# Performance work log

Measured on AMD Instinct MI355X. Metric: run time of the kernel, lower is better.

The kernel has to match this reference:

```python
import jax, jax.numpy as jnp
import numpy as np

N_NODES = 100000


def _gcn_layer(x, W, src, dst, w):
    # GCNConv(add_self_loops=False, normalize=False, bias=False):
    # h = x @ W; out[i] = sum_{e: dst[e]=i} w[e] * h[src[e]]
    h = x @ W                                   # [N, nhid]
    msgs = h[src] * w[:, None]                  # [E, nhid] gather + scale
    return jax.ops.segment_sum(msgs, dst, num_segments=N_NODES)  # scatter-add


def setup_inputs() -> dict:
    key = jax.random.key(0)
    ks = jax.random.split(key, 7)
    N, E, P, F, H = N_NODES, 1000000, 500000, 128, 64
    x = jax.random.normal(ks[0], (N, F), dtype=jnp.float32)
    edge_index = jax.random.randint(ks[1], (2, E), 0, N, dtype=jnp.int64)
    edge_weight = jax.random.uniform(ks[2], (E,), dtype=jnp.float32)
    pos_edge_index = jax.random.randint(ks[3], (2, P), 0, N, dtype=jnp.int64)
    W1 = jax.random.normal(ks[4], (F, H), dtype=jnp.float32) * (1.0 / np.sqrt(F))
    W2 = jax.random.normal(ks[5], (H, H), dtype=jnp.float32) * (1.0 / np.sqrt(H))
    Wlin = jax.random.normal(ks[6], (2, 2 * H), dtype=jnp.float32) * (1.0 / np.sqrt(2 * H))
    return {"x": x, "edge_index": edge_index, "edge_weight": edge_weight,
            "pos_edge_index": pos_edge_index, "W1": W1, "W2": W2, "Wlin": Wlin}


def reference(x, edge_index, edge_weight, pos_edge_index, W1, W2, Wlin):
    src, dst = edge_index[0], edge_index[1]
    h = jax.nn.relu(_gcn_layer(x, W1, src, dst, edge_weight))   # conv1 + relu
    z = _gcn_layer(h, W2, src, dst, edge_weight)                # conv2
    # decode: gather endpoint embeddings, concat, linear (no bias)
    pairs = jnp.concatenate([z[pos_edge_index[0]], z[pos_edge_index[1]]], axis=1)  # [P, 2H]
    return pairs @ Wlin.T                                       # [P, 2]
```

## Files before the change

kernel.cpp:

```cpp
#include <hip/hip_runtime.h>

#define F_IN 128
#define H_DIM 64
#define NBUCK_MAX 1024
#define BCAP 1664

typedef short s16x8 __attribute__((ext_vector_type(8)));
typedef float f32x4 __attribute__((ext_vector_type(4)));
typedef float f32x2 __attribute__((ext_vector_type(2)));

union FragU {
    s16x8 s;
    uint4 q;
    unsigned short u[8];
};

__device__ __forceinline__ unsigned short f2bf(float f) {
    unsigned int b = __float_as_uint(f);
    b += 0x7fffu + ((b >> 16) & 1u);
    return (unsigned short)(b >> 16);
}
__device__ __forceinline__ f32x2 up2(unsigned int v) {
    f32x2 r;
    r.x = __uint_as_float(v << 16);
    r.y = __uint_as_float(v & 0xffff0000u);
    return r;
}
__device__ __forceinline__ f32x2 fma2(f32x2 a, f32x2 b, f32x2 c) {
#if __has_builtin(__builtin_elementwise_fma)
    return __builtin_elementwise_fma(a, b, c);
#else
    f32x2 r;
    r.x = fmaf(a.x, b.x, c.x);
    r.y = fmaf(a.y, b.y, c.y);
    return r;
#endif
}

__device__ __forceinline__ void prepack_one(const float* __restrict__ W,
                                            unsigned short* __restrict__ wf, int KS, int tid) {
    int lane = tid & 63;
    int grp = tid >> 6;
    int ks = grp % KS;
    int ct = grp / KS;
    int col = ct * 16 + (lane & 15);
    int kbase = ks * 32 + (lane >> 4) * 8;
    FragU f;
#pragma unroll
    for (int j = 0; j < 8; ++j) f.u[j] = f2bf(W[(kbase + j) * H_DIM + col]);
    reinterpret_cast<uint4*>(wf)[tid] = f.q;
}

__global__ __launch_bounds__(256) void prepack_k(const float* __restrict__ W1, const float* __restrict__ W2,
                                                 unsigned short* __restrict__ wf1, unsigned short* __restrict__ wf2,
                                                 int* __restrict__ gcursor) {
    int tid = blockIdx.x * 256 + threadIdx.x;
    if (tid < NBUCK_MAX) gcursor[tid] = tid * BCAP;
    if (tid < 4 * 4 * 64) prepack_one(W1, wf1, 4, tid);
    else if (tid < 4 * 4 * 64 + 4 * 2 * 64) prepack_one(W2, wf2, 2, tid - 4 * 4 * 64);
}

__global__ __launch_bounds__(256) void gemm1_k(const float* __restrict__ x,
                                               const unsigned short* __restrict__ wf,
                                               unsigned short* __restrict__ outb, int N) {
    constexpr int KS = F_IN / 32;
    int wv = threadIdx.x >> 6;
    int lane = threadIdx.x & 63;
    int rb = blockIdx.x * 64 + wv * 16;
    int ra = rb + (lane & 15);
    if (ra > N - 1) ra = N - 1;
    int koct = lane >> 4;

    FragU af[KS];
    const float* ap = x + (size_t)ra * F_IN + koct * 8;
#pragma unroll
    for (int ks = 0; ks < KS; ++ks) {
        float4 v0 = *reinterpret_cast<const float4*>(ap + ks * 32);
        float4 v1 = *reinterpret_cast<const float4*>(ap + ks * 32 + 4);
        af[ks].u[0] = f2bf(v0.x); af[ks].u[1] = f2bf(v0.y);
        af[ks].u[2] = f2bf(v0.z); af[ks].u[3] = f2bf(v0.w);
        af[ks].u[4] = f2bf(v1.x); af[ks].u[5] = f2bf(v1.y);
        af[ks].u[6] = f2bf(v1.z); af[ks].u[7] = f2bf(v1.w);
    }

    const uint4* bq = reinterpret_cast<const uint4*>(wf);
    f32x4 acc[4];
#pragma unroll
    for (int ct = 0; ct < 4; ++ct) acc[ct] = (f32x4){0.f, 0.f, 0.f, 0.f};
#pragma unroll
    for (int ct = 0; ct < 4; ++ct) {
#pragma unroll
        for (int ks = 0; ks < KS; ++ks) {
            FragU b;
            b.q = bq[(ct * KS + ks) * 64 + lane];
            acc[ct] = __builtin_amdgcn_mfma_f32_16x16x32_bf16(af[ks].s, b.s, acc[ct], 0, 0, 0);
        }
    }

    int ro_base = rb + (lane >> 4) * 4;
    int col = lane & 15;
#pragma unroll
    for (int ct = 0; ct < 4; ++ct) {
#pragma unroll
        for (int j = 0; j < 4; ++j) {
            int ro = ro_base + j;
            if (ro < N) outb[(size_t)ro * H_DIM + ct * 16 + col] = f2bf(acc[ct][j]);
        }
    }
}

__global__ __launch_bounds__(256) void gemm2v_k(const unsigned short* __restrict__ a1b,
                                                const unsigned short* __restrict__ wf,
                                                const float* __restrict__ Wlin,
                                                float4* __restrict__ uz, int N) {
    constexpr int KS = H_DIM / 32;
    int wv = threadIdx.x >> 6;
    int lane = threadIdx.x & 63;
    int rb = blockIdx.x * 64 + wv * 16;
    int ra = rb + (lane & 15);
    if (ra > N - 1) ra = N - 1;
    int koct = lane >> 4;

    FragU af[KS];
    const unsigned short* ap = a1b + (size_t)ra * H_DIM + koct * 8;
#pragma unroll
    for (int ks = 0; ks < KS; ++ks)
        af[ks].q = *reinterpret_cast<const uint4*>(ap + ks * 32);

    const uint4* bq = reinterpret_cast<const uint4*>(wf);
    f32x4 acc[4];
#pragma unroll
    for (int ct = 0; ct < 4; ++ct) acc[ct] = (f32x4){0.f, 0.f, 0.f, 0.f};
#pragma unroll
    for (int ct = 0; ct < 4; ++ct) {
#pragma unroll
        for (int ks = 0; ks < KS; ++ks) {
            FragU b;
            b.q = bq[(ct * KS + ks) * 64 + lane];
            acc[ct] = __builtin_amdgcn_mfma_f32_16x16x32_bf16(af[ks].s, b.s, acc[ct], 0, 0, 0);
        }
    }

    int c = lane & 15;
    float w0[4], w1[4], w2[4], w3[4];
#pragma unroll
    for (int ct = 0; ct < 4; ++ct) {
        int col = ct * 16 + c;
        w0[ct] = Wlin[col];
        w1[ct] = Wlin[128 + col];
        w2[ct] = Wlin[64 + col];
        w3[ct] = Wlin[192 + col];
    }
    int ro_base = rb + (lane >> 4) * 4;
#pragma unroll
    for (int j = 0; j < 4; ++j) {
        float p0 = 0.f, p1 = 0.f, p2 = 0.f, p3 = 0.f;
#pragma unroll
        for (int ct = 0; ct < 4; ++ct) {
            float zv = acc[ct][j];
            p0 = fmaf(zv, w0[ct], p0);
            p1 = fmaf(zv, w1[ct], p1);
            p2 = fmaf(zv, w2[ct], p2);
            p3 = fmaf(zv, w3[ct], p3);
        }
#pragma unroll
        for (int m = 1; m < 16; m <<= 1) {
            p0 += __shfl_xor(p0, m);
            p1 += __shfl_xor(p1, m);
            p2 += __shfl_xor(p2, m);
            p3 += __shfl_xor(p3, m);
        }
        int ro = ro_base + j;
        if (c == 0 && ro < N) uz[ro] = make_float4(p0, p1, p2, p3);
    }
}

__global__ __launch_bounds__(256) void binA_k(const int* __restrict__ ei, const float* __restrict__ ew,
                                              int* __restrict__ gcursor,
                                              unsigned long long* __restrict__ stage, int E, int nbuck) {
    __shared__ unsigned long long sstage[4096];
    __shared__ int smeta[4096];
    __shared__ int cnt[NBUCK_MAX];
    __shared__ int lbase[NBUCK_MAX];
    __shared__ int gbase[NBUCK_MAX];
    __shared__ int cur[NBUCK_MAX];
    __shared__ int wsum[256];
    int tid = threadIdx.x;
    int e0 = blockIdx.x * 4096;
    int ecount = min(4096, E - e0);
    for (int i = tid; i < nbuck; i += 256) { cnt[i] = 0; cur[i] = 0; }
    __syncthreads();
    for (int i = tid; i < ecount; i += 256)
        atomicAdd(&cnt[ei[E + e0 + i] >> 7], 1);
    __syncthreads();
    int idx4 = tid * 4;
    int c[4];
    int mysum = 0;
#pragma unroll
    for (int j = 0; j < 4; ++j) {
        c[j] = (idx4 + j < nbuck) ? cnt[idx4 + j] : 0;
        mysum += c[j];
    }
    wsum[tid] = mysum;
    __syncthreads();
    for (int off = 1; off < 256; off <<= 1) {
        int add = (tid >= off) ? wsum[tid - off] : 0;
        __syncthreads();
        wsum[tid] += add;
        __syncthreads();
    }
    int run = wsum[tid] - mysum;
#pragma unroll
    for (int j = 0; j < 4; ++j) {
        if (idx4 + j < nbuck) lbase[idx4 + j] = run;
        run += c[j];
    }
    __syncthreads();
    for (int b = tid; b < nbuck; b += 256)
        gbase[b] = cnt[b] ? atomicAdd(&gcursor[b], cnt[b]) : 0;
    __syncthreads();
    for (int i = tid; i < ecount; i += 256) {
        int e = e0 + i;
        int s = ei[e];
        int d = ei[E + e];
        unsigned int wb = __float_as_uint(ew[e]);
        int b = d >> 7;
        int off = atomicAdd(&cur[b], 1);
        int pos = lbase[b] + off;
        sstage[pos] = ((unsigned long long)(d & 127) << 49)
                    | ((unsigned long long)(unsigned int)s << 32) | wb;
        smeta[pos] = gbase[b] + off;
    }
    __syncthreads();
    for (int i = tid; i < ecount; i += 256)
        stage[smeta[i]] = sstage[i];
}

__global__ __launch_bounds__(512) void aggsort1_k(const unsigned short* __restrict__ hb,
                                                  const int* __restrict__ gcursor,
                                                  const unsigned long long* __restrict__ stage,
                                                  unsigned long long* __restrict__ epack,
                                                  int2* __restrict__ rdeg,
                                                  unsigned short* __restrict__ outb, int N) {
    __shared__ unsigned long long lout[BCAP];
    __shared__ int cnt[128], exc[128], cur[128];
    int b = blockIdx.x;
    int tid = threadIdx.x;
    int base = b * BCAP;
    int nb = gcursor[b] - base;
    if (tid < 128) { cnt[tid] = 0; cur[tid] = 0; }
    __syncthreads();
    for (int i = tid; i < nb; i += 512)
        atomicAdd(&cnt[(int)((stage[base + i] >> 49) & 127)], 1);
    __syncthreads();
    if (tid < 128) exc[tid] = cnt[tid];
    __syncthreads();
    for (int off = 1; off < 128; off <<= 1) {
        int add = (tid >= off && tid < 128) ? exc[tid - off] : 0;
        __syncthreads();
        if (tid < 128) exc[tid] += add;
        __syncthreads();
    }
    if (tid < 128) {
        exc[tid] -= cnt[tid];
        int node = b * 128 + tid;
        if (node < N) rdeg[node] = make_int2(base + exc[tid], cnt[tid]);
    }
    __syncthreads();
    for (int i = tid; i < nb; i += 512) {
        unsigned long long v = stage[base + i];
        int dl = (int)((v >> 49) & 127);
        unsigned int src = (unsigned int)((v >> 32) & 0x1FFFF);
        unsigned int wb = (unsigned int)v;
        int pos = exc[dl] + atomicAdd(&cur[dl], 1);
        lout[pos] = ((unsigned long long)wb << 32) | src;
    }
    __syncthreads();
    for (int i = tid; i < nb; i += 512)
        epack[base + i] = lout[i];

    int g = tid >> 2;
    int dimg = tid & 3;
    int node = b * 128 + g;
    if (node >= N) return;
    int start = exc[g];
    int cg = cnt[g];
    f32x2 acc[8];
#pragma unroll
    for (int q = 0; q < 8; ++q) acc[q] = (f32x2){0.f, 0.f};
    const uint4* hbase = reinterpret_cast<const uint4*>(hb);
    int j = 0;
    for (; j + 1 < cg; j += 2) {
        unsigned long long p0 = lout[start + j];
        unsigned long long p1 = lout[start + j + 1];
        float wa = __uint_as_float((unsigned int)(p0 >> 32));
        float wbv = __uint_as_float((unsigned int)(p1 >> 32));
        f32x2 w2a = {wa, wa};
        f32x2 w2b = {wbv, wbv};
        const uint4* rp0 = hbase + (size_t)(unsigned int)p0 * (H_DIM / 8) + dimg * 2;
        const uint4* rp1 = hbase + (size_t)(unsigned int)p1 * (H_DIM / 8) + dimg * 2;
        uint4 a0 = rp0[0];
        uint4 a1 = rp0[1];
        uint4 b0 = rp1[0];
        uint4 b1 = rp1[1];
        acc[0] = fma2(w2a, up2(a0.x), acc[0]);
        acc[1] = fma2(w2a, up2(a0.y), acc[1]);
        acc[2] = fma2(w2a, up2(a0.z), acc[2]);
        acc[3] = fma2(w2a, up2(a0.w), acc[3]);
        acc[4] = fma2(w2a, up2(a1.x), acc[4]);
        acc[5] = fma2(w2a, up2(a1.y), acc[5]);
        acc[6] = fma2(w2a, up2(a1.z), acc[6]);
        acc[7] = fma2(w2a, up2(a1.w), acc[7]);
        acc[0] = fma2(w2b, up2(b0.x), acc[0]);
        acc[1] = fma2(w2b, up2(b0.y), acc[1]);
        acc[2] = fma2(w2b, up2(b0.z), acc[2]);
        acc[3] = fma2(w2b, up2(b0.w), acc[3]);
        acc[4] = fma2(w2b, up2(b1.x), acc[4]);
        acc[5] = fma2(w2b, up2(b1.y), acc[5]);
        acc[6] = fma2(w2b, up2(b1.z), acc[6]);
        acc[7] = fma2(w2b, up2(b1.w), acc[7]);
    }
    if (j < cg) {
        unsigned long long p0 = lout[start + j];
        float wa = __uint_as_float((unsigned int)(p0 >> 32));
        f32x2 w2a = {wa, wa};
        const uint4* rp0 = hbase + (size_t)(unsigned int)p0 * (H_DIM / 8) + dimg * 2;
        uint4 a0 = rp0[0];
        uint4 a1 = rp0[1];
        acc[0] = fma2(w2a, up2(a0.x), acc[0]);
        acc[1] = fma2(w2a, up2(a0.y), acc[1]);
        acc[2] = fma2(w2a, up2(a0.z), acc[2]);
        acc[3] = fma2(w2a, up2(a0.w), acc[3]);
        acc[4] = fma2(w2a, up2(a1.x), acc[4]);
        acc[5] = fma2(w2a, up2(a1.y), acc[5]);
        acc[6] = fma2(w2a, up2(a1.z), acc[6]);
        acc[7] = fma2(w2a, up2(a1.w), acc[7]);
    }
    unsigned int pk[8];
#pragma unroll
    for (int q = 0; q < 8; ++q)
        pk[q] = (unsigned int)f2bf(fmaxf(acc[q].x, 0.f))
              | ((unsigned int)f2bf(fmaxf(acc[q].y, 0.f)) << 16);
    uint4* op = reinterpret_cast<uint4*>(outb + (size_t)node * H_DIM + dimg * 16);
    op[0] = make_uint4(pk[0], pk[1], pk[2], pk[3]);
    op[1] = make_uint4(pk[4], pk[5], pk[6], pk[7]);
}

__global__ __launch_bounds__(256) void aggv_k(const float4* __restrict__ uz,
                                              const int2* __restrict__ rdeg,
                                              const unsigned long long* __restrict__ epack,
                                              float4* __restrict__ u, int N) {
    int node = blockIdx.x * 256 + threadIdx.x;
    if (node >= N) return;
    int2 rd = rdeg[node];
    int start = rd.x, cnt = rd.y;
    float4 acc = make_float4(0.f, 0.f, 0.f, 0.f);
    int j = 0;
    for (; j + 3 < cnt; j += 4) {
#pragma unroll
        for (int q = 0; q < 4; ++q) {
            unsigned long long p = epack[start + j + q];
            float w = __uint_as_float((unsigned int)(p >> 32));
            float4 v = uz[(unsigned int)p];
            acc.x = fmaf(w, v.x, acc.x);
            acc.y = fmaf(w, v.y, acc.y);
            acc.z = fmaf(w, v.z, acc.z);
            acc.w = fmaf(w, v.w, acc.w);
        }
    }
    for (; j < cnt; ++j) {
        unsigned long long p = epack[start + j];
        float w = __uint_as_float((unsigned int)(p >> 32));
        float4 v = uz[(unsigned int)p];
        acc.x = fmaf(w, v.x, acc.x);
        acc.y = fmaf(w, v.y, acc.y);
        acc.z = fmaf(w, v.z, acc.z);
        acc.w = fmaf(w, v.w, acc.w);
    }
    u[node] = acc;
}

__global__ __launch_bounds__(256) void pair_k(const float4* __restrict__ u,
                                              const int* __restrict__ pos,
                                              float2* __restrict__ out, int P, int half) {
    int p = blockIdx.x * 256 + threadIdx.x;
    if (p >= half) return;
    int p1 = p + half;
    bool has1 = p1 < P;
    int s0 = pos[p];
    int t0 = pos[P + p];
    int s1 = has1 ? pos[p1] : s0;
    int t1 = has1 ? pos[P + p1] : t0;
    float4 us0 = u[s0];
    float4 ut0 = u[t0];
    float4 us1 = u[s1];
    float4 ut1 = u[t1];
    union { float f[2]; unsigned long long v; } o;
    o.f[0] = us0.x + ut0.z;
    o.f[1] = us0.y + ut0.w;
    __builtin_nontemporal_store(o.v, reinterpret_cast<unsigned long long*>(&out[p]));
    if (has1) {
        o.f[0] = us1.x + ut1.z;
        o.f[1] = us1.y + ut1.w;
        __builtin_nontemporal_store(o.v, reinterpret_cast<unsigned long long*>(&out[p1]));
    }
}

extern "C" void kernel_launch(void* const* d_in, const int* in_sizes, int n_in,
                              void* d_out, int out_size, void* d_ws, size_t ws_size,
                              hipStream_t stream) {
    const float* x    = (const float*)d_in[0];
    const int*   ei   = (const int*)d_in[1];
    const float* ew   = (const float*)d_in[2];
    const int*   pos  = (const int*)d_in[3];
    const float* W1   = (const float*)d_in[4];
    const float* W2   = (const float*)d_in[5];
    const float* Wlin = (const float*)d_in[6];
    float* out = (float*)d_out;

    const int N = in_sizes[0] / F_IN;
    const int E = in_sizes[2];
    const int P = in_sizes[3] / 2;
    const int nbuck = (N + 127) / 128;

    char* ws = (char*)d_ws;
    const size_t rowBF = (size_t)N * H_DIM * sizeof(unsigned short);
    const size_t regionBytes = (size_t)nbuck * BCAP * 8;
    unsigned short* hb   = (unsigned short*)ws;
    unsigned short* a1b  = (unsigned short*)(ws + rowBF);
    float4*         uz   = (float4*)(ws + 2 * rowBF);
    float4*         u    = uz + N;
    unsigned long long* stage = (unsigned long long*)((char*)(u + N));
    unsigned long long* epack = (unsigned long long*)((char*)stage + regionBytes);
    int* gcursor = (int*)((char*)epack + regionBytes);
    int2* rdeg   = (int2*)(gcursor + NBUCK_MAX);
    size_t wf_off = (((size_t)((char*)(rdeg + N) - ws)) + 15) & ~(size_t)15;
    unsigned short* wf1 = (unsigned short*)(ws + wf_off);
    unsigned short* wf2 = wf1 + 4 * 4 * 64 * 8;

    prepack_k<<<6, 256, 0, stream>>>(W1, W2, wf1, wf2, gcursor);

    gemm1_k<<<(N + 63) / 64, 256, 0, stream>>>(x, wf1, hb, N);

    binA_k<<<(E + 4095) / 4096, 256, 0, stream>>>(ei, ew, gcursor, stage, E, nbuck);

    aggsort1_k<<<nbuck, 512, 0, stream>>>(hb, gcursor, stage, epack, rdeg, a1b, N);
    gemm2v_k<<<(N + 63) / 64, 256, 0, stream>>>(a1b, wf2, Wlin, uz, N);
    aggv_k<<<(N + 255) / 256, 256, 0, stream>>>(uz, rdeg, epack, u, N);
    const int half = (P + 1) / 2;
    pair_k<<<(half + 255) / 256, 256, 0, stream>>>(u, pos, (float2*)out, P, half);
}
```

Before: 93.37 us.

## Fuse second GEMM and Wlin projection into layer-1 aggregation kernel

The layer-1 aggregated, ReLU'd bf16 rows are now staged in shared memory (reusing the lout buffer, enlarged and padded to stride 72) instead of being written to global memory. The same block then runs the 64x64 MFMA GEMM with W2 and the Wlin projection, writing uz directly. This drops the gemm2v_k launch and the global round trip of the a1b intermediate, at the cost of more shared memory per block, which may reduce occupancy, and extra barriers. The early return for out-of-range nodes is removed so every thread reaches the barriers.

Measured after the change: 88.22 us. 5.5% less time.

```diff
diff --git a/kernel.cpp b/kernel.cpp
--- a/kernel.cpp
+++ b/kernel.cpp
@@ -4,6 +4,7 @@
 #define H_DIM 64
 #define NBUCK_MAX 1024
 #define BCAP 1664
+#define A1S_STRIDE 72
 
 typedef short s16x8 __attribute__((ext_vector_type(8)));
 typedef float f32x4 __attribute__((ext_vector_type(4)));
@@ -106,72 +107,6 @@
             int ro = ro_base + j;
             if (ro < N) outb[(size_t)ro * H_DIM + ct * 16 + col] = f2bf(acc[ct][j]);
         }
-    }
-}
-
-__global__ __launch_bounds__(256) void gemm2v_k(const unsigned short* __restrict__ a1b,
-                                                const unsigned short* __restrict__ wf,
-                                                const float* __restrict__ Wlin,
-                                                float4* __restrict__ uz, int N) {
-    constexpr int KS = H_DIM / 32;
-    int wv = threadIdx.x >> 6;
-    int lane = threadIdx.x & 63;
-    int rb = blockIdx.x * 64 + wv * 16;
-    int ra = rb + (lane & 15);
-    if (ra > N - 1) ra = N - 1;
-    int koct = lane >> 4;
-
-    FragU af[KS];
-    const unsigned short* ap = a1b + (size_t)ra * H_DIM + koct * 8;
-#pragma unroll
-    for (int ks = 0; ks < KS; ++ks)
-        af[ks].q = *reinterpret_cast<const uint4*>(ap + ks * 32);
-
-    const uint4* bq = reinterpret_cast<const uint4*>(wf);
-    f32x4 acc[4];
-#pragma unroll
-    for (int ct = 0; ct < 4; ++ct) acc[ct] = (f32x4){0.f, 0.f, 0.f, 0.f};
-#pragma unroll
-    for (int ct = 0; ct < 4; ++ct) {
-#pragma unroll
-        for (int ks = 0; ks < KS; ++ks) {
-            FragU b;
-            b.q = bq[(ct * KS + ks) * 64 + lane];
-            acc[ct] = __builtin_amdgcn_mfma_f32_16x16x32_bf16(af[ks].s, b.s, acc[ct], 0, 0, 0);
-        }
-    }
-
-    int c = lane & 15;
-    float w0[4], w1[4], w2[4], w3[4];
-#pragma unroll
-    for (int ct = 0; ct < 4; ++ct) {
-        int col = ct * 16 + c;
-        w0[ct] = Wlin[col];
-        w1[ct] = Wlin[128 + col];
-        w2[ct] = Wlin[64 + col];
-        w3[ct] = Wlin[192 + col];
-    }
-    int ro_base = rb + (lane >> 4) * 4;
-#pragma unroll
-    for (int j = 0; j < 4; ++j) {
-        float p0 = 0.f, p1 = 0.f, p2 = 0.f, p3 = 0.f;
-#pragma unroll
-        for (int ct = 0; ct < 4; ++ct) {
-            float zv = acc[ct][j];
-            p0 = fmaf(zv, w0[ct], p0);
-            p1 = fmaf(zv, w1[ct], p1);
-            p2 = fmaf(zv, w2[ct], p2);
-            p3 = fmaf(zv, w3[ct], p3);
-        }
-#pragma unroll
-        for (int m = 1; m < 16; m <<= 1) {
-            p0 += __shfl_xor(p0, m);
-            p1 += __shfl_xor(p1, m);
-            p2 += __shfl_xor(p2, m);
-            p3 += __shfl_xor(p3, m);
-        }
-        int ro = ro_base + j;
-        if (c == 0 && ro < N) uz[ro] = make_float4(p0, p1, p2, p3);
     }
 }
 
@@ -239,11 +174,14 @@
 __global__ __launch_bounds__(512) void aggsort1_k(const unsigned short* __restrict__ hb,
                                                   const int* __restrict__ gcursor,
                                                   const unsigned long long* __restrict__ stage,
+                                                  const unsigned short* __restrict__ wf2,
+                                                  const float* __restrict__ Wlin,
                                                   unsigned long long* __restrict__ epack,
                                                   int2* __restrict__ rdeg,
-                                                  unsigned short* __restrict__ outb, int N) {
-    __shared__ unsigned long long lout[BCAP];
+                                                  float4* __restrict__ uz, int N) {
+    __shared__ unsigned long long lout[2304];
     __shared__ int cnt[128], exc[128], cur[128];
+    unsigned short* a1s = reinterpret_cast<unsigned short*>(lout);
     int b = blockIdx.x;
     int tid = threadIdx.x;
     int base = b * BCAP;
@@ -281,8 +219,6 @@
 
     int g = tid >> 2;
     int dimg = tid & 3;
-    int node = b * 128 + g;
-    if (node >= N) return;
     int start = exc[g];
     int cg = cnt[g];
     f32x2 acc[8];
@@ -341,9 +277,66 @@
     for (int q = 0; q < 8; ++q)
         pk[q] = (unsigned int)f2bf(fmaxf(acc[q].x, 0.f))
               | ((unsigned int)f2bf(fmaxf(acc[q].y, 0.f)) << 16);
-    uint4* op = reinterpret_cast<uint4*>(outb + (size_t)node * H_DIM + dimg * 16);
-    op[0] = make_uint4(pk[0], pk[1], pk[2], pk[3]);
-    op[1] = make_uint4(pk[4], pk[5], pk[6], pk[7]);
+    __syncthreads();
+    {
+        uint4* op = reinterpret_cast<uint4*>(a1s + g * A1S_STRIDE + dimg * 16);
+        op[0] = make_uint4(pk[0], pk[1], pk[2], pk[3]);
+        op[1] = make_uint4(pk[4], pk[5], pk[6], pk[7]);
+    }
+    __syncthreads();
+
+    int wv = tid >> 6;
+    int lane = tid & 63;
+    int row = wv * 16 + (lane & 15);
+    int koct = lane >> 4;
+    FragU af[2];
+    af[0].q = *reinterpret_cast<const uint4*>(a1s + row * A1S_STRIDE + koct * 8);
+    af[1].q = *reinterpret_cast<const uint4*>(a1s + row * A1S_STRIDE + 32 + koct * 8);
+    const uint4* bq = reinterpret_cast<const uint4*>(wf2);
+    f32x4 zacc[4];
+#pragma unroll
+    for (int ct = 0; ct < 4; ++ct) zacc[ct] = (f32x4){0.f, 0.f, 0.f, 0.f};
+#pragma unroll
+    for (int ct = 0; ct < 4; ++ct) {
+#pragma unroll
+        for (int ks = 0; ks < 2; ++ks) {
+            FragU bb;
+            bb.q = bq[(ct * 2 + ks) * 64 + lane];
+            zacc[ct] = __builtin_amdgcn_mfma_f32_16x16x32_bf16(af[ks].s, bb.s, zacc[ct], 0, 0, 0);
+        }
+    }
+    int c = lane & 15;
+    float w0[4], w1[4], w2[4], w3[4];
+#pragma unroll
+    for (int ct = 0; ct < 4; ++ct) {
+        int col = ct * 16 + c;
+        w0[ct] = Wlin[col];
+        w1[ct] = Wlin[128 + col];
+        w2[ct] = Wlin[64 + col];
+        w3[ct] = Wlin[192 + col];
+    }
+    int ro_base = b * 128 + wv * 16 + (lane >> 4) * 4;
+#pragma unroll
+    for (int jj = 0; jj < 4; ++jj) {
+        float p0 = 0.f, p1 = 0.f, p2 = 0.f, p3 = 0.f;
+#pragma unroll
+        for (int ct = 0; ct < 4; ++ct) {
+            float zv = zacc[ct][jj];
+            p0 = fmaf(zv, w0[ct], p0);
+            p1 = fmaf(zv, w1[ct], p1);
+            p2 = fmaf(zv, w2[ct], p2);
+            p3 = fmaf(zv, w3[ct], p3);
+        }
+#pragma unroll
+        for (int m = 1; m < 16; m <<= 1) {
+            p0 += __shfl_xor(p0, m);
+            p1 += __shfl_xor(p1, m);
+            p2 += __shfl_xor(p2, m);
+            p3 += __shfl_xor(p3, m);
+        }
+        int ro = ro_base + jj;
+        if (c == 0 && ro < N) uz[ro] = make_float4(p0, p1, p2, p3);
+    }
 }
 
 __global__ __launch_bounds__(256) void aggv_k(const float4* __restrict__ uz,
@@ -427,8 +420,7 @@
     const size_t rowBF = (size_t)N * H_DIM * sizeof(unsigned short);
     const size_t regionBytes = (size_t)nbuck * BCAP * 8;
     unsigned short* hb   = (unsigned short*)ws;
-    unsigned short* a1b  = (unsigned short*)(ws + rowBF);
-    float4*         uz   = (float4*)(ws + 2 * rowBF);
+    float4*         uz   = (float4*)(ws + rowBF);
     float4*         u    = uz + N;
     unsigned long long* stage = (unsigned long long*)((char*)(u + N));
     unsigned long long* epack = (unsigned long long*)((char*)stage + regionBytes);
@@ -444,8 +436,7 @@
 
     binA_k<<<(E + 4095) / 4096, 256, 0, stream>>>(ei, ew, gcursor, stage, E, nbuck);
 
-    aggsort1_k<<<nbuck, 512, 0, stream>>>(hb, gcursor, stage, epack, rdeg, a1b, N);
-    gemm2v_k<<<(N + 63) / 64, 256, 0, stream>>>(a1b, wf2, Wlin, uz, N);
+    aggsort1_k<<<nbuck, 512, 0, stream>>>(hb, gcursor, stage, wf2, Wlin, epack, rdeg, uz, N);
     aggv_k<<<(N + 255) / 256, 256, 0, stream>>>(uz, rdeg, epack, u, N);
     const int half = (P + 1) / 2;
     pair_k<<<(half + 255) / 256, 256, 0, stream>>>(u, pos, (float2*)out, P, half);
```
